# Kernel tuning notes

Measured on AMD Instinct MI355X. Metric: run time of the kernel, lower is better.

## Reference

```python
import jax, jax.numpy as jnp
import numpy as np

K = 20
EPS = 1e-5
NEG_SLOPE = 0.2


def _graph_feature(x, k):
    # x: [B, N, C] -> edge features [B, N, k, 2C]
    xx = jnp.sum(x * x, axis=-1)                       # [B, N]
    inner = jnp.einsum('bnc,bmc->bnm', x, x)           # [B, N, N]
    neg_dist = 2.0 * inner - xx[:, :, None] - xx[:, None, :]
    idx = jax.lax.top_k(neg_dist, k)[1]                # [B, N, k] nearest neighbors
    nbr = jax.vmap(lambda f, i: f[i])(x, idx)          # [B, N, k, C]
    center = jnp.broadcast_to(x[:, :, None, :], nbr.shape)
    return jnp.concatenate([nbr - center, center], axis=-1)


def _bn(y, gamma, beta, axes):
    mu = y.mean(axes, keepdims=True)
    var = y.var(axes, keepdims=True)
    return (y - mu) * jax.lax.rsqrt(var + EPS) * gamma + beta


def _lrelu(y):
    return jnp.where(y > 0, y, NEG_SLOPE * y)


def _edge_block(feat, w, gamma, beta):
    # feat: [B, N, k, Cin], w: [Cout, Cin] (1x1 conv)
    y = jnp.einsum('bnkc,oc->bnko', feat, w)
    y = _lrelu(_bn(y, gamma, beta, (0, 1, 2)))
    return y.max(axis=2)                               # max over k -> [B, N, Cout]


def setup_inputs() -> dict:
    key = jax.random.key(0)
    ks = jax.random.split(key, 8)
    B, N = 16, 2048
    num_features = 128
    x = jax.random.normal(ks[0], (B, N, 3), dtype=jnp.float32)
    s = 0.05
    w1 = jax.random.normal(ks[1], (64, 6), dtype=jnp.float32) * s
    w2 = jax.random.normal(ks[2], (64, 128), dtype=jnp.float32) * s
    w3 = jax.random.normal(ks[3], (128, 128), dtype=jnp.float32) * s
    w4 = jax.random.normal(ks[4], (256, 256), dtype=jnp.float32) * s
    w5 = jax.random.normal(ks[5], (512, 512), dtype=jnp.float32) * s
    we = jax.random.normal(ks[6], (num_features, 512), dtype=jnp.float32) * s
    def gb(c):
        return jnp.ones((c,), jnp.float32), jnp.zeros((c,), jnp.float32)
    g1, b1 = gb(64); g2, b2 = gb(64); g3, b3 = gb(128); g4, b4 = gb(256); g5, b5 = gb(512)
    return dict(x=x, w1=w1, g1=g1, b1=b1, w2=w2, g2=g2, b2=b2, w3=w3, g3=g3, b3=b3,
                w4=w4, g4=g4, b4=b4, w5=w5, g5=g5, b5=b5, we=we)


def reference(x, w1, g1, b1, w2, g2, b2, w3, g3, b3, w4, g4, b4, w5, g5, b5, we):
    # x: [B, N, 3]
    x1 = _edge_block(_graph_feature(x, K), w1, g1, b1)    # [B, N, 64]
    x2 = _edge_block(_graph_feature(x1, K), w2, g2, b2)   # [B, N, 64]
    x3 = _edge_block(_graph_feature(x2, K), w3, g3, b3)   # [B, N, 128]
    x4 = _edge_block(_graph_feature(x3, K), w4, g4, b4)   # [B, N, 256]
    cat = jnp.concatenate([x1, x2, x3, x4], axis=-1)      # [B, N, 512]
    y = jnp.einsum('bnc,oc->bno', cat, w5)                # conv5 (1x1 conv1d)
    y = _lrelu(_bn(y, g5, b5, (0, 1)))
    y = y.max(axis=1)                                     # global max pool -> [B, 512]
    return y @ we.T                                       # embedding -> [B, num_features]
```

## Files before the change

kernel.cpp:

```cpp
#include <hip/hip_runtime.h>
#include <hip/hip_bf16.h>
#include <cstdint>

#define B_ 16
#define N_ 2048
#define KNN_K 20
#define EPS_ 1e-5f
#define SLOPE_ 0.2f
#define IMS 4.8828125e-4f

typedef __attribute__((ext_vector_type(4))) float f32x4;
typedef __attribute__((ext_vector_type(8))) short bf16x8;
typedef __attribute__((ext_vector_type(8))) _Float16 f16x8;

static __device__ __forceinline__ float lrelu(float v){ return v > 0.f ? v : SLOPE_*v; }

static __device__ __forceinline__ unsigned encf(float f){
  unsigned b = __float_as_uint(f);
  return (b & 0x80000000u) ? ~b : (b | 0x80000000u);
}
static __device__ __forceinline__ float decf(unsigned u){
  unsigned b = (u & 0x80000000u) ? (u ^ 0x80000000u) : ~u;
  return __uint_as_float(b);
}
static __device__ __forceinline__ short bfbits(float v){
  __hip_bfloat16 h = __float2bfloat16(v);
  return *reinterpret_cast<short*>(&h);
}
static __device__ __forceinline__ short h16(float v){
  _Float16 h = (_Float16)v;
  return *reinterpret_cast<short*>(&h);
}
static __device__ __forceinline__ float h2f(short s){
  _Float16 h = *reinterpret_cast<_Float16*>(&s);
  return (float)h;
}

template<int C, int CP>
__global__ __launch_bounds__(256) void convert_kernel(const float* __restrict__ f, int lda,
                                                      short* __restrict__ fbf, size_t plane,
                                                      float* __restrict__ xx){
  int wid  = (blockIdx.x * 256 + threadIdx.x) >> 6;
  int lane = threadIdx.x & 63;
  if (wid >= B_*N_) return;
  const float* p = f + (size_t)wid*lda;
  float s = 0.f;
  for (int c = lane; c < CP; c += 64){
    float v = (c < C) ? p[c] : 0.f;
    short h = h16(v);
    short m = h16((v - h2f(h)) * 2048.f);
    size_t o = (size_t)wid*CP + c;
    fbf[o] = h;
    fbf[plane + o] = m;
    s += v*v;
  }
  #pragma unroll
  for (int off=32; off; off>>=1) s += __shfl_down(s, off);
  if (lane==0) xx[wid] = s;
}

template<int CP>
__global__ __launch_bounds__(256, 2) void knn_mfma(const short* __restrict__ fbf, size_t plane,
                                                const float* __restrict__ xx,
                                                float* __restrict__ pval, int* __restrict__ pidx){
  constexpr int SP = CP + 8;
  constexpr int CH = CP/8;
  constexpr int KC = CP/32;
  constexpr int PFH = CP/32;
  constexpr int FMBS = 2*64*SP;
  constexpr bool ALIAS = (FMBS*2 >= 64*65*4);
  constexpr unsigned LDSB = ALIAS ? (unsigned)(FMBS*2) : (unsigned)(FMBS*2 + 64*65*4);
  __shared__ __align__(16) char ldsbuf[LDSB];
  short* fmb = (short*)ldsbuf;
  float* dtile = ALIAS ? (float*)ldsbuf : (float*)(ldsbuf + FMBS*2);
  __shared__ float xn_s[64], xm_s[64];

  int b   = blockIdx.x >> 6;
  int rem = blockIdx.x & 63;
  int n0  = (rem >> 1) << 6;
  int mh  = rem & 1;
  int mbase = mh << 10;
  int tid = threadIdx.x;
  int w    = tid >> 6;
  int lane = tid & 63;
  int fr = lane & 15, hi = lane >> 4;
  int r_loc = lane >> 2, csub = lane & 3;
  int gb = lane & 60;
  int myrow = w*16 + r_loc;
  size_t browoff = (size_t)b * N_;

  f16x8 aH[KC], aM[KC];
  {
    size_t arow = (browoff + n0 + w*16 + fr) * (size_t)CP;
    #pragma unroll
    for (int kc=0; kc<KC; ++kc){
      aH[kc] = *(const f16x8*)&fbf[arow + kc*32 + hi*8];
      aM[kc] = *(const f16x8*)&fbf[plane + arow + kc*32 + hi*8];
    }
  }
  if (tid < 64) xn_s[tid] = xx[browoff + n0 + tid];

  float sv[5]; int si[5];
  #pragma unroll
  for (int j=0;j<5;++j){ sv[j] = -1e30f; si[j] = 0x7FFFFFFF; }

  f16x8 pf[PFH];
  float xmreg = 0.f;
  auto PFLOAD = [&](int mt){
    int m0 = mbase + (mt<<6);
    #pragma unroll
    for (int j=0;j<PFH;++j){
      int i = tid + j*256;
      int r = i/CH, cq = i - r*CH;
      pf[j] = *(const f16x8*)&fbf[(browoff + m0 + r)*(size_t)CP + cq*8];
    }
    if (tid < 64) xmreg = xx[browoff + m0 + tid];
  };
  auto WRITEPF = [&](int mt){
    int m0 = mbase + (mt<<6);
    #pragma unroll
    for (int j=0;j<PFH;++j){
      int i = tid + j*256;
      int r = i/CH, cq = i - r*CH;
      *(f16x8*)&fmb[r*SP + cq*8] = pf[j];
    }
    #pragma unroll
    for (int j=0;j<PFH;++j){
      int i = tid + j*256;
      int r = i/CH, cq = i - r*CH;
      f16x8 v = *(const f16x8*)&fbf[plane + (browoff + m0 + r)*(size_t)CP + cq*8];
      *(f16x8*)&fmb[64*SP + r*SP + cq*8] = v;
    }
    if (tid < 64) xm_s[tid] = xmreg;
  };

  PFLOAD(0);
  WRITEPF(0);
  __syncthreads();

  for (int mt = 0; mt < 16; ++mt){
    int m0 = mbase + (mt << 6);
    if (mt + 1 < 16) PFLOAD(mt + 1);

    f32x4 accH[4], accM[4];
    #pragma unroll
    for (int ct=0; ct<4; ++ct){ accH[ct] = (f32x4){0.f,0.f,0.f,0.f}; accM[ct] = accH[ct]; }
    const short* BH = fmb;
    const short* BM = fmb + 64*SP;
    #pragma unroll
    for (int kc = 0; kc < KC; ++kc){
      #pragma unroll
      for (int ct=0; ct<4; ++ct){
        int boff = (ct*16 + fr)*SP + kc*32 + hi*8;
        f16x8 bh = *(const f16x8*)&BH[boff];
        f16x8 bm = *(const f16x8*)&BM[boff];
        accH[ct] = __builtin_amdgcn_mfma_f32_16x16x32_f16(aH[kc], bh, accH[ct], 0,0,0);
        accM[ct] = __builtin_amdgcn_mfma_f32_16x16x32_f16(aM[kc], bh, accM[ct], 0,0,0);
        accM[ct] = __builtin_amdgcn_mfma_f32_16x16x32_f16(aH[kc], bm, accM[ct], 0,0,0);
      }
    }
    __syncthreads();

    #pragma unroll
    for (int reg=0; reg<4; ++reg){
      int nl = w*16 + hi*4 + reg;
      float xn = xn_s[nl];
      #pragma unroll
      for (int ct=0; ct<4; ++ct)
        dtile[nl*65 + ct*16 + fr] = 2.f*(accH[ct][reg] + IMS*accM[ct][reg]) - xn - xm_s[ct*16 + fr];
    }

    int base = myrow*65 + csub*16;
    float thr = __shfl(sv[4], lane | 3);
    unsigned qm = 0u;
    #pragma unroll
    for (int jj=0; jj<16; ++jj){
      float v = dtile[base + jj];
      qm |= (v > thr) ? (1u << jj) : 0u;
    }
    unsigned long long bal = __ballot(qm != 0u);
    while (bal){
      unsigned nib = (unsigned)((bal >> gb) & 0xFull);
      int leader = nib ? (gb + (int)__builtin_ctz(nib)) : 64;
      int bbit = (int)__builtin_ctz(qm | 0x10000u);
      float mv = dtile[base + (bbit & 15)];
      int mid = m0 + (csub << 4) + bbit;
      float cv = __shfl(mv, leader);
      int   cid = __shfl(mid, leader);
      qm = (lane == leader) ? (qm & (qm - 1u)) : qm;
      int cnt = 0;
      #pragma unroll
      for (int j=0;j<5;++j) cnt += (sv[j] >= cv) ? 1 : 0;
      cnt += __shfl_xor(cnt, 1);
      cnt += __shfl_xor(cnt, 2);
      int pos = nib ? cnt : 20;
      float pv = __shfl_up(sv[4], 1);
      int   pi = __shfl_up(si[4], 1);
      #pragma unroll
      for (int j=0;j<5;++j){
        int g = csub*5 + j;
        float ns = (g < pos) ? sv[j] : ((g == pos) ? cv : pv);
        int   ni = (g < pos) ? si[j] : ((g == pos) ? cid : pi);
        pv = sv[j]; pi = si[j];
        sv[j] = ns; si[j] = ni;
      }
      bal = __ballot(qm != 0u);
    }

    if (mt + 1 < 16){
      if constexpr (ALIAS){
        __syncthreads();
        WRITEPF(mt + 1);
        __syncthreads();
      } else {
        WRITEPF(mt + 1);
        __syncthreads();
      }
    }
  }

  size_t orow = browoff + n0 + myrow;
  float* pvo = pval + (orow*2 + mh)*KNN_K + csub*5;
  int*   pio = pidx + (orow*2 + mh)*KNN_K + csub*5;
  #pragma unroll
  for (int j=0;j<5;++j){ pvo[j] = sv[j]; pio[j] = si[j]; }
}

__global__ __launch_bounds__(256) void knn_merge(const float* __restrict__ pval,
                                                 const int* __restrict__ pidx,
                                                 int* __restrict__ idxout){
  int r = blockIdx.x*256 + threadIdx.x;
  if (r >= B_*N_) return;
  const float* va = pval + (size_t)r*2*KNN_K;
  const float* vb = va + KNN_K;
  const int*   ia = pidx + (size_t)r*2*KNN_K;
  const int*   ib = ia + KNN_K;
  int i=0, j=0;
  #pragma unroll
  for (int t=0;t<KNN_K;++t){
    float a = va[i], bq = vb[j];
    bool ta = (a >= bq);
    idxout[(size_t)r*KNN_K + t] = ta ? ia[i] : ib[j];
    i += ta ? 1 : 0; j += ta ? 0 : 1;
  }
}

template<int CP>
__global__ __launch_bounds__(256) void gemm_pq2(const short* __restrict__ fbf, size_t plane,
                                                const float* __restrict__ Wsrc, int Cin,
                                                float* __restrict__ P, float* __restrict__ Qo, int O){
  constexpr int BK = (CP < 64) ? CP : 64;
  constexpr int SP = BK + 8;
  __shared__ short Ah[64*SP];
  __shared__ short Am[64*SP];
  __shared__ short WAh[64*SP];
  __shared__ short WAm[64*SP];
  __shared__ short WQh[64*SP];
  __shared__ short WQm[64*SP];
  int obl = O >> 6;
  int bo = ((int)blockIdx.x % obl) << 6;
  int bm = ((int)blockIdx.x / obl) << 6;
  int tid = threadIdx.x;
  int w = tid >> 6, lane = tid & 63;
  int fr = lane & 15, hi = lane >> 4;
  f32x4 aPH[4], aPM[4], aQH[4], aQM[4];
  #pragma unroll
  for (int ct=0; ct<4; ++ct){
    aPH[ct] = (f32x4){0.f,0.f,0.f,0.f};
    aPM[ct] = aPH[ct]; aQH[ct] = aPH[ct]; aQM[ct] = aPH[ct];
  }

  for (int k0=0; k0<CP; k0+=BK){
    __syncthreads();
    for (int i=tid; i < 64*(BK/8); i += 256){
      int r = i/(BK/8), cq = i%(BK/8);
      size_t src = ((size_t)bm + r)*CP + k0 + cq*8;
      *(f16x8*)&Ah[r*SP + cq*8] = *(const f16x8*)&fbf[src];
      *(f16x8*)&Am[r*SP + cq*8] = *(const f16x8*)&fbf[plane + src];
    }
    for (int i=tid; i < 64*(BK/8); i += 256){
      int r = i/(BK/8), cq = i%(BK/8);
      f16x8 vah, vam, vqh, vqm;
      #pragma unroll
      for (int e=0;e<8;++e){
        int c = k0 + cq*8 + e;
        float wa = 0.f, wqv = 0.f;
        if (c < Cin){
          wa  = Wsrc[(size_t)(bo + r)*2*Cin + c];
          wqv = Wsrc[(size_t)(bo + r)*2*Cin + Cin + c] - wa;
        }
        _Float16 ha = (_Float16)wa;
        vah[e] = ha;
        vam[e] = (_Float16)((wa - (float)ha) * 2048.f);
        _Float16 hq = (_Float16)wqv;
        vqh[e] = hq;
        vqm[e] = (_Float16)((wqv - (float)hq) * 2048.f);
      }
      *(f16x8*)&WAh[r*SP + cq*8] = vah;
      *(f16x8*)&WAm[r*SP + cq*8] = vam;
      *(f16x8*)&WQh[r*SP + cq*8] = vqh;
      *(f16x8*)&WQm[r*SP + cq*8] = vqm;
    }
    __syncthreads();
    #pragma unroll
    for (int kc=0; kc<BK/32; ++kc){
      f16x8 ah = *(const f16x8*)&Ah[(w*16 + fr)*SP + kc*32 + hi*8];
      f16x8 am = *(const f16x8*)&Am[(w*16 + fr)*SP + kc*32 + hi*8];
      #pragma unroll
      for (int ct=0; ct<4; ++ct){
        int boff = (ct*16 + fr)*SP + kc*32 + hi*8;
        f16x8 bh = *(const f16x8*)&WAh[boff];
        f16x8 bm = *(const f16x8*)&WAm[boff];
        f16x8 qh = *(const f16x8*)&WQh[boff];
        f16x8 qm = *(const f16x8*)&WQm[boff];
        aPH[ct] = __builtin_amdgcn_mfma_f32_16x16x32_f16(ah, bh, aPH[ct], 0,0,0);
        aPM[ct] = __builtin_amdgcn_mfma_f32_16x16x32_f16(am, bh, aPM[ct], 0,0,0);
        aPM[ct] = __builtin_amdgcn_mfma_f32_16x16x32_f16(ah, bm, aPM[ct], 0,0,0);
        aQH[ct] = __builtin_amdgcn_mfma_f32_16x16x32_f16(ah, qh, aQH[ct], 0,0,0);
        aQM[ct] = __builtin_amdgcn_mfma_f32_16x16x32_f16(am, qh, aQM[ct], 0,0,0);
        aQM[ct] = __builtin_amdgcn_mfma_f32_16x16x32_f16(ah, qm, aQM[ct], 0,0,0);
      }
    }
  }
  #pragma unroll
  for (int ct=0; ct<4; ++ct)
    #pragma unroll
    for (int reg=0; reg<4; ++reg){
      int row = bm + w*16 + hi*4 + reg;
      size_t o = (size_t)row*O + bo + ct*16 + fr;
      P[o]  = aPH[ct][reg] + IMS*aPM[ct][reg];
      Qo[o] = aQH[ct][reg] + IMS*aQM[ct][reg];
    }
}

__global__ __launch_bounds__(256) void gemm_bf16_stats(const float* __restrict__ A,
                                                       const float* __restrict__ Wt,
                                                       const float* __restrict__ g5,
                                                       float* __restrict__ sums,
                                                       float* __restrict__ sumsq,
                                                       unsigned* __restrict__ maxenc){
  __shared__ short As[128*72];
  __shared__ short Bs[64*72];
  __shared__ float s1[64], s2[64];
  int bm = (int)(blockIdx.x >> 3) << 7;
  int bo = (int)(blockIdx.x & 7) << 6;
  int tid = threadIdx.x;
  int w = tid >> 6, lane = tid & 63;
  int fr = lane & 15, hi = lane >> 4;
  f32x4 acc[2][4];
  #pragma unroll
  for (int g=0; g<2; ++g)
    #pragma unroll
    for (int ct=0; ct<4; ++ct) acc[g][ct] = (f32x4){0.f,0.f,0.f,0.f};

  for (int k0=0; k0<512; k0+=64){
    __syncthreads();
    #pragma unroll 2
    for (int i = tid; i < 1024; i += 256){
      int r = i >> 3, cq = i & 7;
      const float* src = &A[(size_t)(bm + r)*512 + k0 + cq*8];
      bf16x8 v;
      #pragma unroll
      for (int e=0;e<8;++e) v[e] = bfbits(src[e]);
      *(bf16x8*)&As[r*72 + cq*8] = v;
    }
    #pragma unroll 2
    for (int i = tid; i < 512; i += 256){
      int r = i >> 3, cq = i & 7;
      const float* src = &Wt[(size_t)(bo + r)*512 + k0 + cq*8];
      bf16x8 v;
      #pragma unroll
      for (int e=0;e<8;++e) v[e] = bfbits(src[e]);
      *(bf16x8*)&Bs[r*72 + cq*8] = v;
    }
    __syncthreads();
    #pragma unroll
    for (int kc=0; kc<2; ++kc){
      bf16x8 a0 = *(const bf16x8*)&As[(w*32 +      fr)*72 + kc*32 + hi*8];
      bf16x8 a1 = *(const bf16x8*)&As[(w*32 + 16 + fr)*72 + kc*32 + hi*8];
      #pragma unroll
      for (int ct=0; ct<4; ++ct){
        bf16x8 bb = *(const bf16x8*)&Bs[(ct*16 + fr)*72 + kc*32 + hi*8];
        acc[0][ct] = __builtin_amdgcn_mfma_f32_16x16x32_bf16(a0, bb, acc[0][ct], 0,0,0);
        acc[1][ct] = __builtin_amdgcn_mfma_f32_16x16x32_bf16(a1, bb, acc[1][ct], 0,0,0);
      }
    }
  }

  __syncthreads();
  if (tid < 64){ s1[tid] = 0.f; s2[tid] = 0.f; }
  __syncthreads();
  int bidx = bm >> 11;
  #pragma unroll
  for (int ct=0; ct<4; ++ct){
    int o = bo + ct*16 + fr;
    float ga = g5[o];
    float s = 0.f, ss = 0.f, mx = -1e30f;
    #pragma unroll
    for (int g=0; g<2; ++g)
      #pragma unroll
      for (int reg=0; reg<4; ++reg){
        float v = acc[g][ct][reg];
        s += v; ss += v*v;
        float sel = ga >= 0.f ? v : -v;
        mx = fmaxf(mx, sel);
      }
    s  += __shfl_xor(s, 16);  s  += __shfl_xor(s, 32);
    ss += __shfl_xor(ss, 16); ss += __shfl_xor(ss, 32);
    mx = fmaxf(mx, __shfl_xor(mx, 16)); mx = fmaxf(mx, __shfl_xor(mx, 32));
    if (hi == 0){
      atomicAdd(&s1[ct*16 + fr], s);
      atomicAdd(&s2[ct*16 + fr], ss);
      atomicMax(&maxenc[bidx*512 + o], encf(mx));
    }
  }
  __syncthreads();
  if (tid < 64){
    atomicAdd(&sums[bo + tid],  s1[tid]);
    atomicAdd(&sumsq[bo + tid], s2[tid]);
  }
}

__global__ void zero_f_kernel(float* p, int n){
  int i = blockIdx.x*blockDim.x + threadIdx.x;
  if (i < n) p[i] = 0.f;
}
__global__ void zero_u_kernel(unsigned* p, int n){
  int i = blockIdx.x*blockDim.x + threadIdx.x;
  if (i < n) p[i] = 0u;
}

__global__ __launch_bounds__(256) void edge_agg(const float* __restrict__ P, const float* __restrict__ Q,
      const int* __restrict__ idx, const float* __restrict__ gamma,
      float* __restrict__ S, float* __restrict__ sums, float* __restrict__ sumsq, int O){
  const int ROWS = 64;
  int rpi = 256 / O;
  int iters = ROWS / rpi;
  int row0 = blockIdx.x * ROWS;
  int tid = threadIdx.x;
  int o  = tid % O;
  int rl = tid / O;
  int b  = row0 / N_;
  __shared__ int sidx[4][KNN_K];
  __shared__ float s1[256], s2[256];
  float g = gamma[o];
  float csum=0.f, csumsq=0.f;
  for (int it=0; it<iters; ++it){
    __syncthreads();
    if (tid < KNN_K*rpi) sidx[tid/KNN_K][tid%KNN_K] = idx[(size_t)(row0 + it*rpi)*KNN_K + tid];
    __syncthreads();
    int row = row0 + it*rpi + rl;
    float q = Q[(size_t)row*O + o];
    float mx=-1e30f, mn=1e30f, s=0.f, ss=0.f;
    #pragma unroll
    for (int k=0;k<KNN_K;++k){
      int m = sidx[rl][k];
      float p = P[((size_t)b*N_ + m)*O + o];
      mx = fmaxf(mx,p); mn = fminf(mn,p);
      float y = p + q; s += y; ss += y*y;
    }
    csum += s; csumsq += ss;
    S[(size_t)row*O + o] = (g >= 0.f ? mx : mn) + q;
  }
  s1[tid]=0.f; s2[tid]=0.f;
  __syncthreads();
  atomicAdd(&s1[o], csum); atomicAdd(&s2[o], csumsq);
  __syncthreads();
  if (tid < O){ atomicAdd(&sums[tid], s1[tid]); atomicAdd(&sumsq[tid], s2[tid]); }
}

__global__ void bn_finalize(const float* __restrict__ sums, const float* __restrict__ sumsq,
                            const float* __restrict__ gamma, const float* __restrict__ beta,
                            float invM, float* __restrict__ scale, float* __restrict__ shift, int O){
  int o = blockIdx.x*blockDim.x + threadIdx.x;
  if (o >= O) return;
  float mu = sums[o]*invM;
  float var = sumsq[o]*invM - mu*mu;
  float rs = rsqrtf(var + EPS_);
  float sc = gamma[o]*rs;
  scale[o] = sc; shift[o] = beta[o] - mu*sc;
}

__global__ void apply_write(const float* __restrict__ S, const float* __restrict__ scale,
                            const float* __restrict__ shift, float* __restrict__ cat, int off, int O){
  int i = blockIdx.x*blockDim.x + threadIdx.x;
  if (i >= B_*N_*O) return;
  int row = i / O, o = i - row*O;
  float v = S[i]*scale[o] + shift[o];
  cat[(size_t)row*512 + off + o] = lrelu(v);
}

__global__ void pool_kernel(const unsigned* __restrict__ maxenc, const float* __restrict__ scale,
                            const float* __restrict__ shift, const float* __restrict__ g5,
                            float* __restrict__ pooled){
  int i = blockIdx.x*blockDim.x + threadIdx.x;
  if (i >= B_*512) return;
  int o = i & 511;
  float t = decf(maxenc[i]);
  float y = g5[o] >= 0.f ? t : -t;
  pooled[i] = lrelu(y*scale[o] + shift[o]);
}

__global__ void final_mm(const float* __restrict__ pooled, const float* __restrict__ we,
                         float* __restrict__ out){
  int i = blockIdx.x*blockDim.x + threadIdx.x;
  if (i >= B_*128) return;
  int b = i >> 7, j = i & 127;
  const float4* pp = (const float4*)(pooled + (size_t)b*512);
  const float4* wp = (const float4*)(we + (size_t)j*512);
  float s = 0.f;
  for (int c=0;c<128;++c){
    float4 a = pp[c], w = wp[c];
    s += a.x*w.x + a.y*w.y + a.z*w.z + a.w*w.w;
  }
  out[i] = s;
}

struct Ws {
  float* cat; float* P; float* Q; float* S; int* idx; float* xx;
  float* sums; float* sumsq; float* scale; float* shift;
  unsigned* maxenc; float* pooled; short* fbf;
  float* pval; int* pidx;
};

template<int C, int CP>
static void run_layer(const Ws& W, const float* f, int lda, int O,
                      const float* w, const float* g, const float* bt,
                      int off_out, hipStream_t stream){
  const int M = B_*N_;
  size_t plane = (size_t)M*CP;
  convert_kernel<C, CP><<<M/4, 256, 0, stream>>>(f, lda, W.fbf, plane, W.xx);
  knn_mfma<CP><<<B_*(N_/64)*2, 256, 0, stream>>>(W.fbf, plane, W.xx, W.pval, W.pidx);
  knn_merge<<<(M+255)/256, 256, 0, stream>>>(W.pval, W.pidx, W.idx);
  int grid = (M/64)*(O/64);
  gemm_pq2<CP><<<grid, 256, 0, stream>>>(W.fbf, plane, w, C, W.P, W.Q, O);
  zero_f_kernel<<<4, 256, 0, stream>>>(W.sums, 1024);
  edge_agg<<<M/64, 256, 0, stream>>>(W.P, W.Q, W.idx, g, W.S, W.sums, W.sumsq, O);
  bn_finalize<<<(O+255)/256, 256, 0, stream>>>(W.sums, W.sumsq, g, bt,
                                               1.f/((float)M*KNN_K), W.scale, W.shift, O);
  apply_write<<<(M*O+255)/256, 256, 0, stream>>>(W.S, W.scale, W.shift, W.cat, off_out, O);
}

extern "C" void kernel_launch(void* const* d_in, const int* in_sizes, int n_in,
                              void* d_out, int out_size, void* d_ws, size_t ws_size,
                              hipStream_t stream) {
  const float* x  = (const float*)d_in[0];
  const float* w1 = (const float*)d_in[1];
  const float* g1 = (const float*)d_in[2];
  const float* b1 = (const float*)d_in[3];
  const float* w2 = (const float*)d_in[4];
  const float* g2 = (const float*)d_in[5];
  const float* b2 = (const float*)d_in[6];
  const float* w3 = (const float*)d_in[7];
  const float* g3 = (const float*)d_in[8];
  const float* b3 = (const float*)d_in[9];
  const float* w4 = (const float*)d_in[10];
  const float* g4 = (const float*)d_in[11];
  const float* b4 = (const float*)d_in[12];
  const float* w5 = (const float*)d_in[13];
  const float* g5 = (const float*)d_in[14];
  const float* b5 = (const float*)d_in[15];
  const float* we = (const float*)d_in[16];

  char* ws = (char*)d_ws;
  Ws W;
  size_t off = 0;
  W.cat   = (float*)(ws + off); off += (size_t)16*2048*512*4;
  W.P     = (float*)(ws + off); off += (size_t)16*2048*256*4;
  W.Q     = (float*)(ws + off); off += (size_t)16*2048*256*4;
  W.S     = (float*)(ws + off); off += (size_t)16*2048*256*4;
  W.idx   = (int*)  (ws + off); off += (size_t)16*2048*20*4;
  W.xx    = (float*)(ws + off); off += (size_t)16*2048*4;
  W.sums  = (float*)(ws + off); off += 512*4;
  W.sumsq = (float*)(ws + off); off += 512*4;
  W.scale = (float*)(ws + off); off += 512*4;
  W.shift = (float*)(ws + off); off += 512*4;
  W.maxenc= (unsigned*)(ws + off); off += (size_t)16*512*4;
  W.pooled= (float*)(ws + off); off += (size_t)16*512*4;
  W.fbf   = (short*)W.S;
  W.pval  = W.Q;
  W.pidx  = (int*)(W.Q + (size_t)2*16*2048*KNN_K);

  const int M = B_*N_;

  run_layer<3,   32>(W, x,           3,   64,  w1, g1, b1, 0,   stream);
  run_layer<64,  64>(W, W.cat,       512, 64,  w2, g2, b2, 64,  stream);
  run_layer<64,  64>(W, W.cat + 64,  512, 128, w3, g3, b3, 128, stream);
  run_layer<128,128>(W, W.cat + 128, 512, 256, w4, g4, b4, 256, stream);

  zero_f_kernel<<<4, 256, 0, stream>>>(W.sums, 1024);
  zero_u_kernel<<<32, 256, 0, stream>>>(W.maxenc, 16*512);
  gemm_bf16_stats<<<(M/128)*8, 256, 0, stream>>>(W.cat, w5, g5, W.sums, W.sumsq, W.maxenc);
  bn_finalize<<<2, 256, 0, stream>>>(W.sums, W.sumsq, g5, b5, 1.f/(float)M, W.scale, W.shift, 512);
  pool_kernel<<<(16*512+255)/256, 256, 0, stream>>>(W.maxenc, W.scale, W.shift, g5, W.pooled);
  final_mm<<<(16*128+255)/256, 256, 0, stream>>>(W.pooled, we, (float*)d_out);
}
```

Baseline: 1.162 ms.

## Stream KNN neighbor tiles into LDS via global_load_lds with XOR swizzle

Replaces the register-staged prefetch of neighbor feature tiles (global load into registers, later write to padded LDS) with direct global-to-LDS loads, using an XOR swizzle instead of row padding to avoid bank conflicts. The distance tile now has its own LDS buffer instead of aliasing the feature buffer. The next tile's loads are issued right after the distance tile is written, so they overlap the top-k selection, and one barrier per iteration is removed. In exchange, LDS use grows and the occupancy hint of two blocks per CU is dropped, which may lower occupancy.

```diff
diff --git a/kernel.cpp b/kernel.cpp
--- a/kernel.cpp
+++ b/kernel.cpp
@@ -12,6 +12,9 @@
 typedef __attribute__((ext_vector_type(4))) float f32x4;
 typedef __attribute__((ext_vector_type(8))) short bf16x8;
 typedef __attribute__((ext_vector_type(8))) _Float16 f16x8;
+
+typedef const __attribute__((address_space(1))) void* as1cv;
+typedef __attribute__((address_space(3))) void* as3v;
 
 static __device__ __forceinline__ float lrelu(float v){ return v > 0.f ? v : SLOPE_*v; }
 
@@ -60,19 +63,17 @@
 }
 
 template<int CP>
-__global__ __launch_bounds__(256, 2) void knn_mfma(const short* __restrict__ fbf, size_t plane,
+__global__ __launch_bounds__(256) void knn_mfma(const short* __restrict__ fbf, size_t plane,
                                                 const float* __restrict__ xx,
                                                 float* __restrict__ pval, int* __restrict__ pidx){
-  constexpr int SP = CP + 8;
-  constexpr int CH = CP/8;
   constexpr int KC = CP/32;
-  constexpr int PFH = CP/32;
-  constexpr int FMBS = 2*64*SP;
-  constexpr bool ALIAS = (FMBS*2 >= 64*65*4);
-  constexpr unsigned LDSB = ALIAS ? (unsigned)(FMBS*2) : (unsigned)(FMBS*2 + 64*65*4);
-  __shared__ __align__(16) char ldsbuf[LDSB];
-  short* fmb = (short*)ldsbuf;
-  float* dtile = ALIAS ? (float*)ldsbuf : (float*)(ldsbuf + FMBS*2);
+  constexpr int ROWB = CP*2;
+  constexpr int LPR = ROWB/16;
+  constexpr int RPI = 64/LPR;
+  constexpr int NI  = 64/RPI;
+  constexpr int SMASK = (ROWB/16 >= 8) ? 7 : (ROWB/16 - 1);
+  __shared__ __align__(16) short fmb[2*64*CP];
+  __shared__ float dtile[64*65];
   __shared__ float xn_s[64], xm_s[64];
 
   int b   = blockIdx.x >> 6;
@@ -98,69 +99,65 @@
       aM[kc] = *(const f16x8*)&fbf[plane + arow + kc*32 + hi*8];
     }
   }
-  if (tid < 64) xn_s[tid] = xx[browoff + n0 + tid];
 
   float sv[5]; int si[5];
   #pragma unroll
   for (int j=0;j<5;++j){ sv[j] = -1e30f; si[j] = 0x7FFFFFFF; }
 
-  f16x8 pf[PFH];
+  unsigned lofs[2];
+  {
+    int lsub = tid & 63;
+  }
+  unsigned lo0, lo1;
+  {
+    int rg = lane / LPR;
+    int ib = (lane % LPR) * 16;
+    lo0 = (unsigned)(rg*ROWB + (ib ^ ((rg & SMASK) << 4)));
+    int rg1 = rg + ((RPI == 4) ? 4 : 0);
+    lo1 = (unsigned)(rg*ROWB + (ib ^ ((rg1 & SMASK) << 4)));
+  }
+
+  const char* fbfB = (const char*)fbf;
+  size_t planeB = plane * 2;
+
+  auto GLDS = [&](int mt){
+    size_t baseB = (browoff + mbase + ((size_t)mt << 6)) * (size_t)ROWB;
+    const char* sH = fbfB + baseB;
+    #pragma unroll
+    for (int j = w; j < NI; j += 4){
+      unsigned lo = ((RPI == 4) && (j & 1)) ? lo1 : lo0;
+      const char* srcH = sH + (size_t)j*RPI*ROWB + lo;
+      __builtin_amdgcn_global_load_lds((as1cv)srcH, (as3v)&fmb[j*RPI*CP], 16, 0, 0);
+      __builtin_amdgcn_global_load_lds((as1cv)(srcH + planeB), (as3v)&fmb[64*CP + j*RPI*CP], 16, 0, 0);
+    }
+  };
+
+  GLDS(0);
   float xmreg = 0.f;
-  auto PFLOAD = [&](int mt){
-    int m0 = mbase + (mt<<6);
-    #pragma unroll
-    for (int j=0;j<PFH;++j){
-      int i = tid + j*256;
-      int r = i/CH, cq = i - r*CH;
-      pf[j] = *(const f16x8*)&fbf[(browoff + m0 + r)*(size_t)CP + cq*8];
-    }
-    if (tid < 64) xmreg = xx[browoff + m0 + tid];
-  };
-  auto WRITEPF = [&](int mt){
-    int m0 = mbase + (mt<<6);
-    #pragma unroll
-    for (int j=0;j<PFH;++j){
-      int i = tid + j*256;
-      int r = i/CH, cq = i - r*CH;
-      *(f16x8*)&fmb[r*SP + cq*8] = pf[j];
-    }
-    #pragma unroll
-    for (int j=0;j<PFH;++j){
-      int i = tid + j*256;
-      int r = i/CH, cq = i - r*CH;
-      f16x8 v = *(const f16x8*)&fbf[plane + (browoff + m0 + r)*(size_t)CP + cq*8];
-      *(f16x8*)&fmb[64*SP + r*SP + cq*8] = v;
-    }
-    if (tid < 64) xm_s[tid] = xmreg;
-  };
-
-  PFLOAD(0);
-  WRITEPF(0);
+  if (tid < 64){
+    xn_s[tid] = xx[browoff + n0 + tid];
+    xm_s[tid] = xx[browoff + mbase + tid];
+  }
   __syncthreads();
 
   for (int mt = 0; mt < 16; ++mt){
     int m0 = mbase + (mt << 6);
-    if (mt + 1 < 16) PFLOAD(mt + 1);
 
     f32x4 accH[4], accM[4];
     #pragma unroll
     for (int ct=0; ct<4; ++ct){ accH[ct] = (f32x4){0.f,0.f,0.f,0.f}; accM[ct] = accH[ct]; }
-    const short* BH = fmb;
-    const short* BM = fmb + 64*SP;
     #pragma unroll
     for (int kc = 0; kc < KC; ++kc){
       #pragma unroll
       for (int ct=0; ct<4; ++ct){
-        int boff = (ct*16 + fr)*SP + kc*32 + hi*8;
-        f16x8 bh = *(const f16x8*)&BH[boff];
-        f16x8 bm = *(const f16x8*)&BM[boff];
+        int boff = (ct*16 + fr)*CP + ((((kc*64 + hi*16) ^ ((fr & SMASK) << 4))) >> 1);
+        f16x8 bh = *(const f16x8*)&fmb[boff];
+        f16x8 bm = *(const f16x8*)&fmb[64*CP + boff];
         accH[ct] = __builtin_amdgcn_mfma_f32_16x16x32_f16(aH[kc], bh, accH[ct], 0,0,0);
         accM[ct] = __builtin_amdgcn_mfma_f32_16x16x32_f16(aM[kc], bh, accM[ct], 0,0,0);
         accM[ct] = __builtin_amdgcn_mfma_f32_16x16x32_f16(aH[kc], bm, accM[ct], 0,0,0);
       }
     }
-    __syncthreads();
-
     #pragma unroll
     for (int reg=0; reg<4; ++reg){
       int nl = w*16 + hi*4 + reg;
@@ -168,6 +165,12 @@
       #pragma unroll
       for (int ct=0; ct<4; ++ct)
         dtile[nl*65 + ct*16 + fr] = 2.f*(accH[ct][reg] + IMS*accM[ct][reg]) - xn - xm_s[ct*16 + fr];
+    }
+    __syncthreads();
+
+    if (mt + 1 < 16){
+      GLDS(mt + 1);
+      if (tid < 64) xmreg = xx[browoff + mbase + ((mt+1)<<6) + tid];
     }
 
     int base = myrow*65 + csub*16;
@@ -208,14 +211,8 @@
     }
 
     if (mt + 1 < 16){
-      if constexpr (ALIAS){
-        __syncthreads();
-        WRITEPF(mt + 1);
-        __syncthreads();
-      } else {
-        WRITEPF(mt + 1);
-        __syncthreads();
-      }
+      if (tid < 64) xm_s[tid] = xmreg;
+      __syncthreads();
     }
   }
 
```

After: 1.225 ms. 5.4% more time.
